# Performance work log

Hardware: AMD Instinct MI355X
Metric: run time of the kernel (lower is better)

The kernel has to match this reference:

```python
import jax, jax.numpy as jnp
import numpy as np

COMMITMENT_COST = 0.25  # hardcoded in VQVAEModel (quantizer commitment_cost=0.25)


def setup_inputs() -> dict:
    key = jax.random.key(0)
    k1, k2 = jax.random.split(key)
    B, D, H, W = 128, 64, 32, 32
    K = 512
    inputs = jax.random.normal(k1, (B, D, H, W), dtype=jnp.float32)
    codebook = jax.random.normal(k2, (K, D), dtype=jnp.float32)  # nn.Embedding weight, normal_()
    return {"inputs": inputs, "codebook": codebook}


def reference(inputs, codebook):
    # VectorQuantizerEMA.forward in eval mode (no EMA buffer update).
    B, D, H, W = inputs.shape
    K = codebook.shape[0]
    # BCHW -> BHWC
    x = jnp.transpose(inputs, (0, 2, 3, 1))
    flat = x.reshape(-1, D)  # [N, D], N = B*H*W
    distances = (jnp.sum(flat * flat, axis=1, keepdims=True)
                 + jnp.sum(codebook * codebook, axis=1)
                 - 2.0 * flat @ codebook.T)
    # max_one_hot(-distances) == one-hot of argmin(distances)
    idx = jnp.argmin(distances, axis=1)  # [N]
    oh = jax.nn.one_hot(idx, K, dtype=flat.dtype)  # [N, K]
    # quantized = onehot @ codebook (detached) == gather, same math, cheaper
    quantized = jax.lax.stop_gradient(codebook[idx]).reshape(x.shape)  # [B,H,W,D]
    # commitment loss (quantized is detached under torch.no_grad)
    e_latent_loss = jnp.mean((quantized - x) ** 2)
    loss = COMMITMENT_COST * e_latent_loss
    # straight-through estimator
    q_st = x + jax.lax.stop_gradient(quantized - x)
    # perplexity of codebook usage
    avg_probs = jnp.mean(oh, axis=0)
    perplexity = jnp.exp(-jnp.sum(avg_probs * jnp.log(avg_probs + 1e-10)))
    # oh_encodings: rearrange '(b n) d -> b d n'
    oh_encodings = jnp.transpose(oh.reshape(B, H * W, K), (0, 2, 1))  # [B, K, N]
    quantized_out = jnp.transpose(q_st, (0, 3, 1, 2))  # back to BCHW
    return loss, quantized_out, perplexity, oh_encodings
```

## Files before the change

kernel.cpp:

```cpp
#include <hip/hip_runtime.h>
#include <hip/hip_bf16.h>
#include <float.h>

#define NB 128
#define DD 64
#define HH 32
#define WW 32
#define NTOT (NB*HH*WW)
#define KC 512
#define HWSZ 1024

#define OFF_LOSS  0
#define OFF_QUANT 1
#define OFF_PERP  8388609
#define OFF_OH    8388610

#define WS_COUNTS 1
#define WS_ENORM  1024
#define WS_IDX    2048

__global__ __launch_bounds__(256)
void vq_prep(const float* __restrict__ cb, float* __restrict__ ws) {
    int t = blockIdx.x * 256 + threadIdx.x;
    if (t == 0) ws[0] = 0.0f;
    ((int*)ws)[WS_COUNTS + t] = 0;
    const float4* row = (const float4*)(cb + (t << 6));
    float s = 0.0f;
#pragma unroll
    for (int i = 0; i < 16; ++i) {
        float4 v = row[i];
        s = fmaf(v.x, v.x, s); s = fmaf(v.y, v.y, s);
        s = fmaf(v.z, v.z, s); s = fmaf(v.w, v.w, s);
    }
    ws[WS_ENORM + t] = s;
}

#define TILE_K 128
#define EU_LD  65

__global__ __launch_bounds__(256)
void vq_argmin(const float* __restrict__ x, const float* __restrict__ cb,
               const float* __restrict__ ws, int* __restrict__ idx_out,
               int* __restrict__ counts, float* __restrict__ loss_acc) {
    __shared__ float smem[4096 + TILE_K*EU_LD + 64 + 64];
    float (*Xs)[64]    = (float(*)[64])smem;
    float (*Eu)[EU_LD] = (float(*)[EU_LD])(smem + 4096);
    float* xn  = smem + 4096 + TILE_K*EU_LD;
    float* wls = xn + 64;
    float* redv1 = smem + 4096;
    int*   redi1 = (int*)(redv1 + 1024);
    float* redv2 = redv1 + 2048;
    int*   redi2 = (int*)(redv1 + 3072);

    const float* enorm = ws + WS_ENORM;
    int t  = threadIdx.x;
    int wg = blockIdx.x;
    int n0 = wg * 64;
    int b  = n0 >> 10;
    int sp0 = n0 & 1023;
    const float* xbase = x + ((size_t)b << 16) + sp0;

#pragma unroll
    for (int i = 0; i < 4; ++i) {
        int e4 = i * 256 + t;
        int d  = e4 >> 4;
        int r4 = (e4 & 15) << 2;
        float4 v = *(const float4*)(xbase + (size_t)d * 1024 + r4);
        *(float4*)&Xs[d][r4] = v;
    }
    __syncthreads();

    if (t < 64) {
        float s = 0.0f;
        for (int d = 0; d < 64; ++d) { float v = Xs[d][t]; s = fmaf(v, v, s); }
        xn[t] = s;
    }

    int tr = t >> 4, tc = t & 15;
    int rb = tr << 2;

    float v1[4], v2[4];
    int   i1[4], i2[4];
#pragma unroll
    for (int i = 0; i < 4; ++i) { v1[i] = FLT_MAX; v2[i] = FLT_MAX; i1[i] = 0; i2[i] = 0; }

    for (int kt = 0; kt < 4; ++kt) {
        int k0 = kt * TILE_K;
        __syncthreads();
#pragma unroll
        for (int i = 0; i < 8; ++i) {
            int f  = i * 256 + t;
            int k  = f >> 4;
            int d4 = (f & 15) << 2;
            float4 v = *(const float4*)(cb + (size_t)(k0 + k) * 64 + d4);
            Eu[k][d4+0] = v.x; Eu[k][d4+1] = v.y; Eu[k][d4+2] = v.z; Eu[k][d4+3] = v.w;
        }
        __syncthreads();

        float acc[4][8];
#pragma unroll
        for (int i = 0; i < 4; ++i)
#pragma unroll
            for (int j = 0; j < 8; ++j) acc[i][j] = 0.0f;

#pragma unroll 8
        for (int d = 0; d < 64; ++d) {
            float4 xa = *(const float4*)&Xs[d][rb];
            float ev[8];
#pragma unroll
            for (int j = 0; j < 8; ++j) ev[j] = Eu[tc + 16*j][d];
#pragma unroll
            for (int j = 0; j < 8; ++j) {
                acc[0][j] = fmaf(xa.x, ev[j], acc[0][j]);
                acc[1][j] = fmaf(xa.y, ev[j], acc[1][j]);
                acc[2][j] = fmaf(xa.z, ev[j], acc[2][j]);
                acc[3][j] = fmaf(xa.w, ev[j], acc[3][j]);
            }
        }

#pragma unroll
        for (int j = 0; j < 8; ++j) {
            int k = k0 + tc + 16*j;
            float en = enorm[k];
#pragma unroll
            for (int i = 0; i < 4; ++i) {
                float s = fmaf(-2.0f, acc[i][j], en);
                if (s < v1[i]) { v2[i] = v1[i]; i2[i] = i1[i]; v1[i] = s; i1[i] = k; }
                else if (s < v2[i]) { v2[i] = s; i2[i] = k; }
            }
        }
    }

    __syncthreads();
#pragma unroll
    for (int i = 0; i < 4; ++i) {
        redv1[tc*64 + rb + i] = v1[i];
        redi1[tc*64 + rb + i] = i1[i];
        redv2[tc*64 + rb + i] = v2[i];
        redi2[tc*64 + rb + i] = i2[i];
    }
    __syncthreads();

    if (t < 64) {
        float V1 = FLT_MAX, V2 = FLT_MAX;
        int   I1 = 0x7fffffff, I2 = 0x7fffffff;
        for (int c = 0; c < 16; ++c) {
            float a1 = redv1[c*64 + t]; int j1 = redi1[c*64 + t];
            float a2 = redv2[c*64 + t]; int j2 = redi2[c*64 + t];
            if (a1 < V1 || (a1 == V1 && j1 < I1)) {
                V2 = V1; I2 = I1; V1 = a1; I1 = j1;
            } else if (a1 < V2) { V2 = a1; I2 = j1; }
            if (a2 < V2) { V2 = a2; I2 = j2; }
        }
        float mind;
        if (V2 - V1 < 5e-3f) {
            const float* c1 = cb + ((size_t)I1 << 6);
            const float* c2 = cb + ((size_t)I2 << 6);
            double d1 = 0.0, d2 = 0.0;
            for (int d = 0; d < 64; ++d) {
                double xv = (double)Xs[d][t];
                double t1 = xv - (double)c1[d];
                double t2 = xv - (double)c2[d];
                d1 += t1*t1; d2 += t2*t2;
            }
            if (d2 < d1 || (d2 == d1 && I2 < I1)) { I1 = I2; mind = (float)d2; }
            else mind = (float)d1;
        } else {
            mind = xn[t] + V1;
        }
        idx_out[n0 + t] = I1;
        atomicAdd(&counts[I1], 1);
        wls[t] = mind;
    }
    __syncthreads();
    if (t == 0) {
        float s = 0.0f;
        for (int r = 0; r < 64; ++r) s += wls[r];
        atomicAdd(loss_acc, s);
    }
}

__global__ __launch_bounds__(256)
void vq_quant(const float* __restrict__ cb, const int* __restrict__ idx,
              float* __restrict__ qout) {
    int n = blockIdx.x * 256 + threadIdx.x;
    int b = n >> 10, sp = n & 1023;
    int k = idx[n];
    const float4* row = (const float4*)(cb + ((size_t)k << 6));
    float* obase = qout + (((size_t)b << 6) << 10) + sp;
#pragma unroll
    for (int d4 = 0; d4 < 16; ++d4) {
        float4 v = row[d4];
        obase[(size_t)(4*d4 + 0) * 1024] = v.x;
        obase[(size_t)(4*d4 + 1) * 1024] = v.y;
        obase[(size_t)(4*d4 + 2) * 1024] = v.z;
        obase[(size_t)(4*d4 + 3) * 1024] = v.w;
    }
}

__global__ __launch_bounds__(256)
void vq_onehot(const int* __restrict__ idx, float* __restrict__ oh) {
    int tid = blockIdx.x * 256 + threadIdx.x;
    int e0 = tid << 2;
    int sp = e0 & 1023;
    int bk = e0 >> 10;
    int k  = bk & 511;
    int b  = bk >> 9;
    int4 iv = *(const int4*)(idx + (b << 10) + sp);
    float2 lo = { iv.x == k ? 1.0f : 0.0f, iv.y == k ? 1.0f : 0.0f };
    float2 hi = { iv.z == k ? 1.0f : 0.0f, iv.w == k ? 1.0f : 0.0f };
    float* p = oh + e0;
    *(float2*)p = lo;
    *(float2*)(p + 2) = hi;
}

__global__ __launch_bounds__(512)
void vq_final(const float* __restrict__ ws, float* __restrict__ out) {
    __shared__ float sh[512];
    int t = threadIdx.x;
    const int* counts = (const int*)ws + WS_COUNTS;
    float p = (float)counts[t] * (1.0f / (float)NTOT);
    sh[t] = p * logf(p + 1e-10f);
    __syncthreads();
    for (int s = 256; s > 0; s >>= 1) {
        if (t < s) sh[t] += sh[t + s];
        __syncthreads();
    }
    if (t == 0) {
        out[OFF_PERP] = expf(-sh[0]);
        out[OFF_LOSS] = 0.25f * ws[0] / ((float)NTOT * 64.0f);
    }
}

extern "C" void kernel_launch(void* const* d_in, const int* in_sizes, int n_in,
                              void* d_out, int out_size, void* d_ws, size_t ws_size,
                              hipStream_t stream) {
    const float* x  = (const float*)d_in[0];
    const float* cb = (const float*)d_in[1];
    float* out = (float*)d_out;
    float* ws  = (float*)d_ws;

    float* loss_acc = ws;
    int*   counts   = (int*)ws + WS_COUNTS;
    int*   idx      = (int*)ws + WS_IDX;
    float* qout     = out + OFF_QUANT;
    float* oh       = out + OFF_OH;

    vq_prep  <<<2,     256, 0, stream>>>(cb, ws);
    vq_argmin<<<NTOT/64, 256, 0, stream>>>(x, cb, ws, idx, counts, loss_acc);
    vq_quant <<<NTOT/256, 256, 0, stream>>>(cb, idx, qout);
    vq_onehot<<<(67108864/4)/256, 256, 0, stream>>>(idx, oh);
    vq_final <<<1,     512, 0, stream>>>(ws, out);
}
```

Baseline: 510.3 us.

## Compute VQ distances with split-bf16 MFMA and exact recheck of near ties

Replaces the fp32 FMA distance GEMM with bf16 MFMA instructions, splitting x and codebook into hi/lo bf16 parts so three products approximate fp32 precision. Codebook halves are precomputed once into scratch space in the one-hot output region, which the later one-hot kernel overwrites. Points whose best and second-best distances fall within a tolerance are flagged and re-evaluated by a new kernel that does an exact double-precision scan over all codes, fixing counts and loss. This cuts ALU cost of the argmin stage but adds a kernel launch and risks mismatched indices if the tolerance misses ties.

```diff
diff --git a/kernel.cpp b/kernel.cpp
--- a/kernel.cpp
+++ b/kernel.cpp
@@ -4,179 +4,253 @@
 
 #define NB 128
 #define DD 64
-#define HH 32
-#define WW 32
-#define NTOT (NB*HH*WW)
+#define NTOT (NB*32*32)
 #define KC 512
-#define HWSZ 1024
 
 #define OFF_LOSS  0
 #define OFF_QUANT 1
 #define OFF_PERP  8388609
 #define OFF_OH    8388610
 
+#define EHI_F  8388612
+#define ELO_F  (EHI_F + 16384)
+#define DIST_F (ELO_F + 16384)
+
 #define WS_COUNTS 1
 #define WS_ENORM  1024
 #define WS_IDX    2048
 
-__global__ __launch_bounds__(256)
-void vq_prep(const float* __restrict__ cb, float* __restrict__ ws) {
+#define FLAG_BIT  (1 << 16)
+#define TAU       1.5e-3f
+
+typedef __attribute__((ext_vector_type(8))) short short8;
+typedef __attribute__((ext_vector_type(4))) float f32x4;
+
+__device__ inline unsigned short f2bf(float f) {
+    unsigned u = __builtin_bit_cast(unsigned, f);
+    unsigned r = (u + 0x7fffu + ((u >> 16) & 1u)) >> 16;
+    return (unsigned short)r;
+}
+__device__ inline float bf2f(unsigned short h) {
+    return __builtin_bit_cast(float, ((unsigned)h) << 16);
+}
+
+__global__ __launch_bounds__(256)
+void vq_prep(const float* __restrict__ cb, float* __restrict__ ws,
+             float* __restrict__ out) {
     int t = blockIdx.x * 256 + threadIdx.x;
     if (t == 0) ws[0] = 0.0f;
     ((int*)ws)[WS_COUNTS + t] = 0;
-    const float4* row = (const float4*)(cb + (t << 6));
-    float s = 0.0f;
-#pragma unroll
-    for (int i = 0; i < 16; ++i) {
-        float4 v = row[i];
-        s = fmaf(v.x, v.x, s); s = fmaf(v.y, v.y, s);
-        s = fmaf(v.z, v.z, s); s = fmaf(v.w, v.w, s);
-    }
-    ws[WS_ENORM + t] = s;
-}
-
-#define TILE_K 128
-#define EU_LD  65
-
-__global__ __launch_bounds__(256)
-void vq_argmin(const float* __restrict__ x, const float* __restrict__ cb,
-               const float* __restrict__ ws, int* __restrict__ idx_out,
-               int* __restrict__ counts, float* __restrict__ loss_acc) {
-    __shared__ float smem[4096 + TILE_K*EU_LD + 64 + 64];
-    float (*Xs)[64]    = (float(*)[64])smem;
-    float (*Eu)[EU_LD] = (float(*)[EU_LD])(smem + 4096);
-    float* xn  = smem + 4096 + TILE_K*EU_LD;
-    float* wls = xn + 64;
-    float* redv1 = smem + 4096;
-    int*   redi1 = (int*)(redv1 + 1024);
-    float* redv2 = redv1 + 2048;
-    int*   redi2 = (int*)(redv1 + 3072);
-
-    const float* enorm = ws + WS_ENORM;
-    int t  = threadIdx.x;
-    int wg = blockIdx.x;
-    int n0 = wg * 64;
+    short* ehi = (short*)(out + EHI_F);
+    short* elo = (short*)(out + ELO_F);
+    const float* row = cb + (t << 6);
+    double s = 0.0;
+#pragma unroll
+    for (int j = 0; j < 8; ++j) {
+        float4 a = *(const float4*)(row + j*8);
+        float4 b = *(const float4*)(row + j*8 + 4);
+        float v[8] = {a.x,a.y,a.z,a.w,b.x,b.y,b.z,b.w};
+        short8 h8, l8;
+#pragma unroll
+        for (int e = 0; e < 8; ++e) {
+            s += (double)v[e] * (double)v[e];
+            unsigned short h = f2bf(v[e]);
+            float hf = bf2f(h);
+            unsigned short l = f2bf(v[e] - hf);
+            h8[e] = (short)h; l8[e] = (short)l;
+        }
+        *(short8*)(ehi + (t << 6) + j*8) = h8;
+        *(short8*)(elo + (t << 6) + j*8) = l8;
+    }
+    ws[WS_ENORM + t] = (float)s;
+}
+
+__global__ __launch_bounds__(256)
+void vq_argmin(const float* __restrict__ x, const float* __restrict__ ws_enorm,
+               const float* __restrict__ out_scratch,
+               int* __restrict__ idx_out, int* __restrict__ counts,
+               float* __restrict__ loss_acc, float* __restrict__ dist_out) {
+    __shared__ __align__(16) short Xh[8][2][4][16][8];
+    __shared__ __align__(16) short Xl[8][2][4][16][8];
+    __shared__ float en_s[512];
+    __shared__ float xn_s[128];
+
+    int t = threadIdx.x;
+    int n0 = blockIdx.x * 128;
     int b  = n0 >> 10;
     int sp0 = n0 & 1023;
     const float* xbase = x + ((size_t)b << 16) + sp0;
 
 #pragma unroll
-    for (int i = 0; i < 4; ++i) {
+    for (int i = 0; i < 8; ++i) {
         int e4 = i * 256 + t;
-        int d  = e4 >> 4;
-        int r4 = (e4 & 15) << 2;
-        float4 v = *(const float4*)(xbase + (size_t)d * 1024 + r4);
-        *(float4*)&Xs[d][r4] = v;
-    }
+        int d  = e4 >> 5;
+        int r4 = (e4 & 31) << 2;
+        float4 v4 = *(const float4*)(xbase + (size_t)d * 1024 + r4);
+        float v[4] = {v4.x, v4.y, v4.z, v4.w};
+        int ks = d >> 5, g = (d >> 3) & 3, dj = d & 7;
+#pragma unroll
+        for (int j = 0; j < 4; ++j) {
+            int r = r4 + j;
+            unsigned short h = f2bf(v[j]);
+            float hf = bf2f(h);
+            unsigned short l = f2bf(v[j] - hf);
+            Xh[r >> 4][ks][g][r & 15][dj] = (short)h;
+            Xl[r >> 4][ks][g][r & 15][dj] = (short)l;
+        }
+    }
+    en_s[t]       = ws_enorm[t];
+    en_s[t + 256] = ws_enorm[t + 256];
     __syncthreads();
 
-    if (t < 64) {
+    if (t < 128) {
         float s = 0.0f;
-        for (int d = 0; d < 64; ++d) { float v = Xs[d][t]; s = fmaf(v, v, s); }
-        xn[t] = s;
-    }
-
-    int tr = t >> 4, tc = t & 15;
-    int rb = tr << 2;
-
-    float v1[4], v2[4];
-    int   i1[4], i2[4];
-#pragma unroll
-    for (int i = 0; i < 4; ++i) { v1[i] = FLT_MAX; v2[i] = FLT_MAX; i1[i] = 0; i2[i] = 0; }
-
-    for (int kt = 0; kt < 4; ++kt) {
-        int k0 = kt * TILE_K;
-        __syncthreads();
-#pragma unroll
-        for (int i = 0; i < 8; ++i) {
-            int f  = i * 256 + t;
-            int k  = f >> 4;
-            int d4 = (f & 15) << 2;
-            float4 v = *(const float4*)(cb + (size_t)(k0 + k) * 64 + d4);
-            Eu[k][d4+0] = v.x; Eu[k][d4+1] = v.y; Eu[k][d4+2] = v.z; Eu[k][d4+3] = v.w;
-        }
-        __syncthreads();
-
-        float acc[4][8];
-#pragma unroll
-        for (int i = 0; i < 4; ++i)
-#pragma unroll
-            for (int j = 0; j < 8; ++j) acc[i][j] = 0.0f;
-
-#pragma unroll 8
-        for (int d = 0; d < 64; ++d) {
-            float4 xa = *(const float4*)&Xs[d][rb];
-            float ev[8];
-#pragma unroll
-            for (int j = 0; j < 8; ++j) ev[j] = Eu[tc + 16*j][d];
-#pragma unroll
-            for (int j = 0; j < 8; ++j) {
-                acc[0][j] = fmaf(xa.x, ev[j], acc[0][j]);
-                acc[1][j] = fmaf(xa.y, ev[j], acc[1][j]);
-                acc[2][j] = fmaf(xa.z, ev[j], acc[2][j]);
-                acc[3][j] = fmaf(xa.w, ev[j], acc[3][j]);
+        int xt = t >> 4, c = t & 15;
+#pragma unroll
+        for (int ks = 0; ks < 2; ++ks)
+#pragma unroll
+            for (int g = 0; g < 4; ++g) {
+                short8 h8 = *(const short8*)&Xh[xt][ks][g][c][0];
+                short8 l8 = *(const short8*)&Xl[xt][ks][g][c][0];
+#pragma unroll
+                for (int e = 0; e < 8; ++e) {
+                    float xv = bf2f((unsigned short)h8[e]) + bf2f((unsigned short)l8[e]);
+                    s = fmaf(xv, xv, s);
+                }
             }
-        }
-
-#pragma unroll
-        for (int j = 0; j < 8; ++j) {
-            int k = k0 + tc + 16*j;
-            float en = enorm[k];
-#pragma unroll
-            for (int i = 0; i < 4; ++i) {
-                float s = fmaf(-2.0f, acc[i][j], en);
-                if (s < v1[i]) { v2[i] = v1[i]; i2[i] = i1[i]; v1[i] = s; i1[i] = k; }
-                else if (s < v2[i]) { v2[i] = s; i2[i] = k; }
+        xn_s[t] = s;
+    }
+    __syncthreads();
+
+    int w = t >> 6, lane = t & 63;
+    int c = lane & 15, g = lane >> 4;
+
+    short8 bh[2][2], bl[2][2];
+#pragma unroll
+    for (int xl_ = 0; xl_ < 2; ++xl_) {
+        int xt = w * 2 + xl_;
+#pragma unroll
+        for (int ks = 0; ks < 2; ++ks) {
+            bh[xl_][ks] = *(const short8*)&Xh[xt][ks][g][c][0];
+            bl[xl_][ks] = *(const short8*)&Xl[xt][ks][g][c][0];
+        }
+    }
+
+    const short* pAh = (const short*)(out_scratch + EHI_F) + (c << 6) + (g << 3);
+    const short* pAl = (const short*)(out_scratch + ELO_F) + (c << 6) + (g << 3);
+
+    float v1[2] = {FLT_MAX, FLT_MAX}, v2[2] = {FLT_MAX, FLT_MAX};
+    int   i1[2] = {0, 0},            i2[2] = {0, 0};
+
+#pragma unroll 2
+    for (int kt = 0; kt < 32; ++kt) {
+        short8 ah0 = *(const short8*)(pAh + (kt << 10));
+        short8 ah1 = *(const short8*)(pAh + (kt << 10) + 32);
+        short8 al0 = *(const short8*)(pAl + (kt << 10));
+        short8 al1 = *(const short8*)(pAl + (kt << 10) + 32);
+        float4 en4 = *(const float4*)&en_s[(kt << 4) + (g << 2)];
+#pragma unroll
+        for (int xl_ = 0; xl_ < 2; ++xl_) {
+            f32x4 acc = {0.f, 0.f, 0.f, 0.f};
+            acc = __builtin_amdgcn_mfma_f32_16x16x32_bf16(ah0, bh[xl_][0], acc, 0, 0, 0);
+            acc = __builtin_amdgcn_mfma_f32_16x16x32_bf16(ah1, bh[xl_][1], acc, 0, 0, 0);
+            acc = __builtin_amdgcn_mfma_f32_16x16x32_bf16(al0, bh[xl_][0], acc, 0, 0, 0);
+            acc = __builtin_amdgcn_mfma_f32_16x16x32_bf16(al1, bh[xl_][1], acc, 0, 0, 0);
+            acc = __builtin_amdgcn_mfma_f32_16x16x32_bf16(ah0, bl[xl_][0], acc, 0, 0, 0);
+            acc = __builtin_amdgcn_mfma_f32_16x16x32_bf16(ah1, bl[xl_][1], acc, 0, 0, 0);
+            float en_[4] = {en4.x, en4.y, en4.z, en4.w};
+#pragma unroll
+            for (int r = 0; r < 4; ++r) {
+                float dd = fmaf(-2.0f, acc[r], en_[r]);
+                int k = (kt << 4) + (g << 2) + r;
+                bool lt1 = dd < v1[xl_];
+                bool lt2 = dd < v2[xl_];
+                v2[xl_] = lt1 ? v1[xl_] : (lt2 ? dd : v2[xl_]);
+                i2[xl_] = lt1 ? i1[xl_] : (lt2 ? k  : i2[xl_]);
+                v1[xl_] = lt1 ? dd : v1[xl_];
+                i1[xl_] = lt1 ? k  : i1[xl_];
             }
         }
     }
 
-    __syncthreads();
-#pragma unroll
-    for (int i = 0; i < 4; ++i) {
-        redv1[tc*64 + rb + i] = v1[i];
-        redi1[tc*64 + rb + i] = i1[i];
-        redv2[tc*64 + rb + i] = v2[i];
-        redi2[tc*64 + rb + i] = i2[i];
-    }
-    __syncthreads();
-
-    if (t < 64) {
-        float V1 = FLT_MAX, V2 = FLT_MAX;
-        int   I1 = 0x7fffffff, I2 = 0x7fffffff;
-        for (int c = 0; c < 16; ++c) {
-            float a1 = redv1[c*64 + t]; int j1 = redi1[c*64 + t];
-            float a2 = redv2[c*64 + t]; int j2 = redi2[c*64 + t];
-            if (a1 < V1 || (a1 == V1 && j1 < I1)) {
-                V2 = V1; I2 = I1; V1 = a1; I1 = j1;
-            } else if (a1 < V2) { V2 = a1; I2 = j1; }
-            if (a2 < V2) { V2 = a2; I2 = j2; }
-        }
-        float mind;
-        if (V2 - V1 < 5e-3f) {
-            const float* c1 = cb + ((size_t)I1 << 6);
-            const float* c2 = cb + ((size_t)I2 << 6);
-            double d1 = 0.0, d2 = 0.0;
+    float dmin[2];
+#pragma unroll
+    for (int xl_ = 0; xl_ < 2; ++xl_) {
+        float V1 = v1[xl_], V2 = v2[xl_]; int I1 = i1[xl_], I2 = i2[xl_];
+#pragma unroll
+        for (int off = 16; off <= 32; off <<= 1) {
+            float o1 = __shfl_xor(V1, off); int oi1 = __shfl_xor(I1, off);
+            float o2 = __shfl_xor(V2, off); int oi2 = __shfl_xor(I2, off);
+            if (o1 < V1 || (o1 == V1 && oi1 < I1)) {
+                V2 = V1; I2 = I1; V1 = o1; I1 = oi1;
+            } else if (o1 < V2 || (o1 == V2 && oi1 < I2)) { V2 = o1; I2 = oi1; }
+            if (o2 < V2 || (o2 == V2 && oi2 < I2)) { V2 = o2; I2 = oi2; }
+        }
+        v1[xl_] = V1; i1[xl_] = I1; v2[xl_] = V2;
+        dmin[xl_] = 0.f;
+        if (g == 0) {
+            int xt = w * 2 + xl_;
+            int n  = n0 + xt * 16 + c;
+            int flag = (V2 - V1 < TAU) ? FLAG_BIT : 0;
+            idx_out[n] = I1 | flag;
+            float dm = xn_s[xt * 16 + c] + V1;
+            dist_out[n] = dm;
+            atomicAdd(&counts[I1], 1);
+            dmin[xl_] = dm;
+        }
+    }
+    float contrib = dmin[0] + dmin[1];
+#pragma unroll
+    for (int off = 1; off <= 8; off <<= 1) contrib += __shfl_xor(contrib, off);
+    if (lane == 0) atomicAdd(loss_acc, contrib);
+}
+
+__global__ __launch_bounds__(256)
+void vq_recheck(const float* __restrict__ x, const float* __restrict__ cb,
+                int* __restrict__ idx_arr, int* __restrict__ counts,
+                float* __restrict__ loss_acc, const float* __restrict__ dist_arr) {
+    int wid  = blockIdx.x * 4 + (threadIdx.x >> 6);
+    int lane = threadIdx.x & 63;
+    int n0 = wid << 6;
+    int iv = idx_arr[n0 + lane];
+    bool fl = (iv & FLAG_BIT) != 0;
+    unsigned long long m = __ballot(fl);
+    int my_old = iv & 511;
+    while (m) {
+        int r = __ffsll((long long)m) - 1; m &= m - 1;
+        int n = n0 + r;
+        int oldi = __shfl(my_old, r);
+        int bb = n >> 10, sp = n & 1023;
+        float xd = x[((size_t)bb << 16) + ((size_t)lane << 10) + sp];
+        double bestd = 1e300; int besti = 0x7fffffff;
+#pragma unroll 2
+        for (int kk = 0; kk < 8; ++kk) {
+            int k = (lane << 3) + kk;
+            const float* er = cb + ((size_t)k << 6);
+            double s = 0.0;
             for (int d = 0; d < 64; ++d) {
-                double xv = (double)Xs[d][t];
-                double t1 = xv - (double)c1[d];
-                double t2 = xv - (double)c2[d];
-                d1 += t1*t1; d2 += t2*t2;
+                float xv = __shfl(xd, d);
+                double df = (double)xv - (double)er[d];
+                s = fma(df, df, s);
             }
-            if (d2 < d1 || (d2 == d1 && I2 < I1)) { I1 = I2; mind = (float)d2; }
-            else mind = (float)d1;
-        } else {
-            mind = xn[t] + V1;
-        }
-        idx_out[n0 + t] = I1;
-        atomicAdd(&counts[I1], 1);
-        wls[t] = mind;
-    }
-    __syncthreads();
-    if (t == 0) {
-        float s = 0.0f;
-        for (int r = 0; r < 64; ++r) s += wls[r];
-        atomicAdd(loss_acc, s);
+            if (s < bestd || (s == bestd && k < besti)) { bestd = s; besti = k; }
+        }
+#pragma unroll
+        for (int off = 32; off; off >>= 1) {
+            double od = __shfl_xor(bestd, off);
+            int    oi = __shfl_xor(besti, off);
+            if (od < bestd || (od == bestd && oi < besti)) { bestd = od; besti = oi; }
+        }
+        if (lane == 0) {
+            if (besti != oldi) {
+                atomicSub(&counts[oldi], 1);
+                atomicAdd(&counts[besti], 1);
+                idx_arr[n] = besti;
+                atomicAdd(loss_acc, (float)bestd - dist_arr[n]);
+            } else {
+                idx_arr[n] = oldi;
+            }
+        }
     }
 }
 
@@ -242,13 +316,16 @@
 
     float* loss_acc = ws;
     int*   counts   = (int*)ws + WS_COUNTS;
+    float* enorm    = ws + WS_ENORM;
     int*   idx      = (int*)ws + WS_IDX;
     float* qout     = out + OFF_QUANT;
     float* oh       = out + OFF_OH;
-
-    vq_prep  <<<2,     256, 0, stream>>>(cb, ws);
-    vq_argmin<<<NTOT/64, 256, 0, stream>>>(x, cb, ws, idx, counts, loss_acc);
-    vq_quant <<<NTOT/256, 256, 0, stream>>>(cb, idx, qout);
-    vq_onehot<<<(67108864/4)/256, 256, 0, stream>>>(idx, oh);
-    vq_final <<<1,     512, 0, stream>>>(ws, out);
-}
+    float* dist     = out + DIST_F;
+
+    vq_prep   <<<2,        256, 0, stream>>>(cb, ws, out);
+    vq_argmin <<<NTOT/128, 256, 0, stream>>>(x, enorm, out, idx, counts, loss_acc, dist);
+    vq_recheck<<<512,      256, 0, stream>>>(x, cb, idx, counts, loss_acc, dist);
+    vq_quant  <<<NTOT/256, 256, 0, stream>>>(cb, idx, qout);
+    vq_onehot <<<(67108864/4)/256, 256, 0, stream>>>(idx, oh);
+    vq_final  <<<1,        512, 0, stream>>>(ws, out);
+}
```

Measured after the change: 520.7 us. 1.02x slower.
